# Performance work log

Hardware: AMD Instinct MI355X
Metric: run time of the kernel (lower is better)

The kernel has to match this reference:

```python
import jax, jax.numpy as jnp
import numpy as np

DIM = 128
N_VAR = 100000
N_CON = 100000
N_NODES = 200000
N_EDGES = 640000


def setup_inputs() -> dict:
    key = jax.random.key(0)
    ks = jax.random.split(key, 25)
    d = DIM
    u = lambda k, s: jax.random.uniform(k, s, jnp.float32, -0.1, 0.1)
    inp = {
        "var_node_features": jax.random.normal(ks[0], (N_VAR, 2), jnp.float32),
        "con_node_features": jax.random.normal(ks[1], (N_CON, 2), jnp.float32),
        "node_types": jax.random.randint(ks[2], (N_NODES,), 0, 2),
        "assoc_var": jnp.arange(N_VAR),
        "assoc_con": N_VAR + jnp.arange(N_CON),
        "edge_index": jax.random.randint(ks[3], (2, N_EDGES), 0, N_NODES),
        "edge_types": jax.random.randint(ks[4], (N_EDGES,), 0, 2),
        "edge_features": jax.random.normal(ks[5], (N_EDGES, 1), jnp.float32),
        "var_w1": u(ks[6], (2, d)), "var_b1": u(ks[7], (d,)),
        "var_w2": u(ks[8], (d, d)), "var_b2": u(ks[9], (d,)),
        "con_w1": u(ks[10], (2, d)), "con_b1": u(ks[11], (d,)),
        "con_w2": u(ks[12], (d, d)), "con_b2": u(ks[13], (d,)),
    }
    for i, k0 in zip((1, 2, 3), (14, 17, 20)):
        inp[f"basis{i}"] = u(ks[k0], (1, d, d))      # num_bases=1
        inp[f"att{i}"] = u(ks[k0 + 1], (2, 1))       # num_relations=2
        inp[f"root{i}"] = u(ks[k0 + 2], (d, d))
        inp[f"bias{i}"] = jnp.zeros((d,), jnp.float32)
    inp["fc1_w"] = u(ks[23], (4 * d, d))
    inp["fc1_b"] = jnp.zeros((d,), jnp.float32)
    inp["fc4_w"] = u(ks[24], (d, 1))
    inp["fc4_b"] = jnp.zeros((1,), jnp.float32)
    return inp


def rgcn(x, src, dst, etype, basis, att, root, bias):
    # basis: [1, d, d], att: [2, 1] -> per-relation weights [2, d, d]
    d = x.shape[-1]
    w = (att @ basis.reshape(basis.shape[0], -1)).reshape(2, d, d)
    xj = x[src]  # [E, d] gather
    # only 2 relations: two GEMMs + select (avoids [E,d,d] materialization)
    msg = jnp.where((etype == 0)[:, None], xj @ w[0], xj @ w[1])
    s = jax.ops.segment_sum(msg, dst, num_segments=N_NODES)
    cnt = jax.ops.segment_sum(jnp.ones((dst.shape[0],), x.dtype), dst, num_segments=N_NODES)
    agg = s / jnp.maximum(cnt, 1.0)[:, None]  # mean aggregation
    return agg + x @ root + bias


def reference(var_node_features, con_node_features, node_types, assoc_var, assoc_con,
              edge_index, edge_types, edge_features,
              var_w1, var_b1, var_w2, var_b2,
              con_w1, con_b1, con_w2, con_b2,
              basis1, att1, root1, bias1,
              basis2, att2, root2, bias2,
              basis3, att3, root3, bias3,
              fc1_w, fc1_b, fc4_w, fc4_b):
    n = jnp.maximum(var_node_features @ var_w1 + var_b1, 0.0) @ var_w2 + var_b2
    e = jnp.maximum(con_node_features @ con_w1 + con_b1, 0.0) @ con_w2 + con_b2
    x = jnp.zeros((node_types.shape[0], n.shape[-1]), n.dtype)
    x = x.at[assoc_var].set(n).at[assoc_con].set(e)
    src, dst = edge_index[0], edge_index[1]
    x1 = jax.nn.relu(rgcn(x, src, dst, edge_types, basis1, att1, root1, bias1))
    x2 = jax.nn.relu(rgcn(x1, src, dst, edge_types, basis2, att2, root2, bias2))
    x3 = jax.nn.relu(rgcn(x2, src, dst, edge_types, basis3, att3, root3, bias3))
    h = jnp.concatenate([x, x1, x2, x3], axis=-1)[assoc_var]  # [n_var, 4d]
    h = jax.nn.relu(h @ fc1_w + fc1_b)
    # dropout p=0.5 is identity in eval mode
    return (h @ fc4_w + fc4_b)[:, 0]
```

## Files before the change

kernel.cpp:

```cpp
#include <hip/hip_runtime.h>
#include <hip/hip_bf16.h>

#define D 128
#define NV 100000
#define NC 100000
#define NN 200000
#define NE 640000

typedef __attribute__((ext_vector_type(4))) float f32x4;
typedef __attribute__((ext_vector_type(8))) short bf16x8;

static __device__ __forceinline__ unsigned short f2b(float f) {
    __hip_bfloat16 h = __float2bfloat16(f);
    union { __hip_bfloat16 h; unsigned short u; } c; c.h = h; return c.u;
}
static __device__ __forceinline__ float b2f(unsigned short b) {
    union { unsigned int u; float f; } c; c.u = ((unsigned int)b) << 16; return c.f;
}

template<bool RELU>
static __device__ __forceinline__ void split8v(const float f[8], bf16x8& ah, bf16x8& al)
{
    union { unsigned short s[8]; bf16x8 v; } ph, pl;
    #pragma unroll
    for (int j = 0; j < 8; ++j) {
        float x = RELU ? fmaxf(f[j], 0.f) : f[j];
        ph.s[j] = f2b(x);
        pl.s[j] = f2b(x - b2f(ph.s[j]));
    }
    ah = ph.v; al = pl.v;
}

union H8 { _Float16 h[8]; uint4 u; };
union H4 { _Float16 h[4]; uint2 u; };

struct PrepArgs { const float* src[12]; };

__global__ __launch_bounds__(256, 1) void prep_kernel(PrepArgs a, unsigned short* wt)
{
    const float* W = a.src[blockIdx.y];
    unsigned short* hi = wt + (size_t)blockIdx.y * 32768;
    unsigned short* lo = hi + 16384;
    const int o = blockIdx.x * 1024 + threadIdx.x * 4;
    const int slice = o >> 10;
    const int n     = (o >> 3) & 127;
    const int j0    = o & 7;
    union { unsigned short s[4]; unsigned long long u; } ph, pl;
    #pragma unroll
    for (int i = 0; i < 4; ++i) {
        const int k = slice * 8 + j0 + i;
        const float w = W[k * 128 + n];
        ph.s[i] = f2b(w);
        pl.s[i] = f2b(w - b2f(ph.s[i]));
    }
    *(unsigned long long*)&hi[o] = ph.u;
    *(unsigned long long*)&lo[o] = pl.u;
}

static __device__ __forceinline__ const bf16x8* wfrag(const unsigned short* wt,
                                                      int ks, int lg, int n)
{
    return (const bf16x8*)(wt + (((ks * 4 + lg) * 128) + n) * 8);
}

static __device__ __forceinline__ char* haddr(char* base, int row, int byteoff)
{
    return base + row * 256 + (byteoff ^ ((row & 7) << 4));
}

template<bool RELU, bool HASAGG>
static __device__ __forceinline__ void wsplit8(uint4 xv, uint4 gv,
                                               char* hb, char* lb, int srow, int ob0)
{
    H8 a0; a0.u = xv;
    float f[8];
    #pragma unroll
    for (int j = 0; j < 8; ++j) f[j] = (float)a0.h[j];
    if (HASAGG) {
        H8 g0; g0.u = gv;
        #pragma unroll
        for (int j = 0; j < 8; ++j) f[j] += (float)g0.h[j];
    }
    bf16x8 h0, l0;
    split8v<RELU>(f, h0, l0);
    *(bf16x8*)(hb + srow * 256 + ob0) = h0;
    *(bf16x8*)(lb + srow * 256 + ob0) = l0;
}

template<int AMODE, bool RELU_A, bool ADD_C>
__global__ __launch_bounds__(256, 4) void gemm6(
    const void* A, const _Float16* __restrict__ agg,
    const float* __restrict__ w1, const float* __restrict__ b1, int M,
    const unsigned short* __restrict__ wt, const float* __restrict__ bias,
    _Float16* Cout)
{
    __shared__ unsigned short Hs[2][2][32 * 128];
    const int tid  = threadIdx.x;
    const int lane = tid & 63, wv = tid >> 6;
    const int li   = lane & 15, lg = lane >> 4;
    const int colbase = wv * 32;

    bf16x8 bh[4][2], bl[4][2];
    #pragma unroll
    for (int ks = 0; ks < 4; ++ks)
        #pragma unroll
        for (int nf = 0; nf < 2; ++nf) {
            const int n = colbase + nf * 16 + li;
            bh[ks][nf] = *wfrag(wt,         ks, lg, n);
            bl[ks][nf] = *wfrag(wt + 16384, ks, lg, n);
        }

    const int ntiles = (M + 31) / 32;
    const int G = gridDim.x;
    const int t0 = blockIdx.x;
    if (t0 >= ntiles) return;

    const int srow = tid >> 3;
    const int skf  = (tid & 7) * 16;
    const int sw   = (srow & 7) << 4;
    const int ob0  = (skf * 2) ^ sw;
    const int ob1  = (skf * 2 + 16) ^ sw;

    #define LOADT(TT, XV0, XV1, GV0, GV1, FV)                                    \
    {                                                                            \
        int grow = (TT) * 32 + srow; if (grow >= M) grow = M - 1;                \
        if (AMODE == 2) {                                                        \
            FV = *(const float2*)((const float*)A + (size_t)grow * 2);           \
        } else {                                                                 \
            const uint4* ap = (const uint4*)((const _Float16*)A + (size_t)grow * D + skf); \
            XV0 = ap[0]; XV1 = ap[1];                                            \
            if (AMODE == 1) {                                                    \
                const uint4* gp = (const uint4*)(agg + (size_t)grow * D + skf);  \
                GV0 = gp[0]; GV1 = gp[1];                                        \
            }                                                                    \
        }                                                                        \
    }
    #define WRITET(BUF, XV0, XV1, GV0, GV1, FV)                                  \
    {                                                                            \
        char* hb_ = (char*)&Hs[BUF][0][0];                                       \
        char* lb_ = (char*)&Hs[BUF][1][0];                                       \
        if (AMODE == 2) {                                                        \
            float f[16];                                                         \
            const float f0 = FV.x, f1 = FV.y;                                    \
            _Pragma("unroll")                                                    \
            for (int q = 0; q < 4; ++q) {                                        \
                const float4 wa = *(const float4*)(w1 + skf + q * 4);            \
                const float4 wb = *(const float4*)(w1 + 128 + skf + q * 4);      \
                const float4 bb = *(const float4*)(b1 + skf + q * 4);            \
                f[q*4+0] = fmaxf(fmaf(f0, wa.x, fmaf(f1, wb.x, bb.x)), 0.f);     \
                f[q*4+1] = fmaxf(fmaf(f0, wa.y, fmaf(f1, wb.y, bb.y)), 0.f);     \
                f[q*4+2] = fmaxf(fmaf(f0, wa.z, fmaf(f1, wb.z, bb.z)), 0.f);     \
                f[q*4+3] = fmaxf(fmaf(f0, wa.w, fmaf(f1, wb.w, bb.w)), 0.f);     \
            }                                                                    \
            bf16x8 h0, l0, h1, l1;                                               \
            split8v<RELU_A>(&f[0], h0, l0);                                     \
            split8v<RELU_A>(&f[8], h1, l1);                                     \
            char* hbr = hb_ + srow * 256; char* lbr = lb_ + srow * 256;          \
            *(bf16x8*)(hbr + ob0) = h0; *(bf16x8*)(hbr + ob1) = h1;              \
            *(bf16x8*)(lbr + ob0) = l0; *(bf16x8*)(lbr + ob1) = l1;              \
        } else {                                                                 \
            wsplit8<RELU_A, AMODE == 1>(XV0, GV0, hb_, lb_, srow, ob0);          \
            wsplit8<RELU_A, AMODE == 1>(XV1, GV1, hb_, lb_, srow, ob1);          \
        }                                                                        \
    }

    {
        uint4 xv0 = {0,0,0,0}, xv1 = {0,0,0,0}, gv0 = {0,0,0,0}, gv1 = {0,0,0,0};
        float2 fv = {0, 0};
        LOADT(t0, xv0, xv1, gv0, gv1, fv);
        WRITET(0, xv0, xv1, gv0, gv1, fv);
    }
    __syncthreads();

    int cur = 0;
    for (int t = t0; t < ntiles; t += G) {
        const int tn = t + G;
        const bool pf = tn < ntiles;
        uint4 xv0 = {0,0,0,0}, xv1 = {0,0,0,0}, gv0 = {0,0,0,0}, gv1 = {0,0,0,0};
        float2 fv = {0, 0};
        if (pf) LOADT(tn, xv0, xv1, gv0, gv1, fv);

        char* hb = (char*)&Hs[cur][0][0];
        char* lb = (char*)&Hs[cur][1][0];
        f32x4 acc[2][2];
        #pragma unroll
        for (int ms = 0; ms < 2; ++ms)
            #pragma unroll
            for (int nf = 0; nf < 2; ++nf) acc[ms][nf] = (f32x4){0.f, 0.f, 0.f, 0.f};
        #pragma unroll
        for (int ks = 0; ks < 4; ++ks) {
            const int kb = ks * 64 + lg * 16;
            bf16x8 ah[2], al[2];
            #pragma unroll
            for (int ms = 0; ms < 2; ++ms) {
                const int row = ms * 16 + li;
                ah[ms] = *(const bf16x8*)haddr(hb, row, kb);
                al[ms] = *(const bf16x8*)haddr(lb, row, kb);
            }
            #pragma unroll
            for (int nf = 0; nf < 2; ++nf)
                #pragma unroll
                for (int ms = 0; ms < 2; ++ms) {
                    acc[ms][nf] = __builtin_amdgcn_mfma_f32_16x16x32_bf16(bh[ks][nf], ah[ms], acc[ms][nf], 0, 0, 0);
                    acc[ms][nf] = __builtin_amdgcn_mfma_f32_16x16x32_bf16(bh[ks][nf], al[ms], acc[ms][nf], 0, 0, 0);
                    acc[ms][nf] = __builtin_amdgcn_mfma_f32_16x16x32_bf16(bl[ks][nf], ah[ms], acc[ms][nf], 0, 0, 0);
                }
        }

        #pragma unroll
        for (int ms = 0; ms < 2; ++ms) {
            const int grow = t * 32 + ms * 16 + li;
            if (grow < M) {
                _Float16* crow = Cout + (size_t)grow * D;
                #pragma unroll
                for (int nf = 0; nf < 2; ++nf) {
                    const int c0 = colbase + nf * 16 + lg * 4;
                    float v[4];
                    #pragma unroll
                    for (int r = 0; r < 4; ++r) v[r] = acc[ms][nf][r];
                    if (bias) {
                        const float4 b = *(const float4*)(bias + c0);
                        v[0] += b.x; v[1] += b.y; v[2] += b.z; v[3] += b.w;
                    }
                    if (ADD_C) {
                        H4 rd; rd.u = *(const uint2*)(crow + c0);
                        #pragma unroll
                        for (int r = 0; r < 4; ++r) v[r] += (float)rd.h[r];
                    }
                    H4 pk;
                    #pragma unroll
                    for (int r = 0; r < 4; ++r) pk.h[r] = (_Float16)v[r];
                    *(uint2*)(crow + c0) = pk.u;
                }
            }
        }

        if (pf) WRITET(cur ^ 1, xv0, xv1, gv0, gv1, fv);
        __syncthreads();
        cur ^= 1;
    }
    #undef LOADT
    #undef WRITET
}

__global__ __launch_bounds__(256, 4) void ugemmf(
    const _Float16* __restrict__ x, const _Float16* __restrict__ agg,
    const _Float16* __restrict__ u, int M,
    const unsigned short* __restrict__ wt,
    const float* __restrict__ fc1_b, const float* __restrict__ fc4_w,
    const float* __restrict__ fc4_b, float* __restrict__ out)
{
    __shared__ unsigned short Hs[2][2][32 * 128];
    const int tid  = threadIdx.x;
    const int lane = tid & 63, wv = tid >> 6;
    const int li   = lane & 15, lg = lane >> 4;
    const int colbase = wv * 32;
    const float fb40 = fc4_b[0];

    bf16x8 bh[4][2], bl[4][2];
    #pragma unroll
    for (int ks = 0; ks < 4; ++ks)
        #pragma unroll
        for (int nf = 0; nf < 2; ++nf) {
            const int n = colbase + nf * 16 + li;
            bh[ks][nf] = *wfrag(wt,         ks, lg, n);
            bl[ks][nf] = *wfrag(wt + 16384, ks, lg, n);
        }

    const int ntiles = (M + 31) / 32;
    const int G = gridDim.x;
    const int t0 = blockIdx.x;
    if (t0 >= ntiles) return;

    const int srow = tid >> 3;
    const int skf  = (tid & 7) * 16;
    const int sw   = (srow & 7) << 4;
    const int ob0  = (skf * 2) ^ sw;
    const int ob1  = (skf * 2 + 16) ^ sw;

    #define LOADU(TT, XV0, XV1, GV0, GV1)                                        \
    {                                                                            \
        int grow = (TT) * 32 + srow; if (grow >= M) grow = M - 1;                \
        const uint4* ap = (const uint4*)(x + (size_t)grow * D + skf);            \
        XV0 = ap[0]; XV1 = ap[1];                                                \
        const uint4* gp = (const uint4*)(agg + (size_t)grow * D + skf);          \
        GV0 = gp[0]; GV1 = gp[1];                                                \
    }

    {
        uint4 xv0, xv1, gv0, gv1;
        LOADU(t0, xv0, xv1, gv0, gv1);
        wsplit8<true, true>(xv0, gv0, (char*)&Hs[0][0][0], (char*)&Hs[0][1][0], srow, ob0);
        wsplit8<true, true>(xv1, gv1, (char*)&Hs[0][0][0], (char*)&Hs[0][1][0], srow, ob1);
    }
    __syncthreads();

    int cur = 0;
    for (int t = t0; t < ntiles; t += G) {
        const int tn = t + G;
        const bool pf = tn < ntiles;
        uint4 xv0 = {0,0,0,0}, xv1 = {0,0,0,0}, gv0 = {0,0,0,0}, gv1 = {0,0,0,0};
        if (pf) LOADU(tn, xv0, xv1, gv0, gv1);

        char* hb = (char*)&Hs[cur][0][0];
        char* lb = (char*)&Hs[cur][1][0];
        f32x4 acc[2][2];
        #pragma unroll
        for (int ms = 0; ms < 2; ++ms)
            #pragma unroll
            for (int nf = 0; nf < 2; ++nf) acc[ms][nf] = (f32x4){0.f, 0.f, 0.f, 0.f};
        #pragma unroll
        for (int ks = 0; ks < 4; ++ks) {
            const int kb = ks * 64 + lg * 16;
            bf16x8 ah[2], al[2];
            #pragma unroll
            for (int ms = 0; ms < 2; ++ms) {
                const int row = ms * 16 + li;
                ah[ms] = *(const bf16x8*)haddr(hb, row, kb);
                al[ms] = *(const bf16x8*)haddr(lb, row, kb);
            }
            #pragma unroll
            for (int nf = 0; nf < 2; ++nf)
                #pragma unroll
                for (int ms = 0; ms < 2; ++ms) {
                    acc[ms][nf] = __builtin_amdgcn_mfma_f32_16x16x32_bf16(bh[ks][nf], ah[ms], acc[ms][nf], 0, 0, 0);
                    acc[ms][nf] = __builtin_amdgcn_mfma_f32_16x16x32_bf16(bh[ks][nf], al[ms], acc[ms][nf], 0, 0, 0);
                    acc[ms][nf] = __builtin_amdgcn_mfma_f32_16x16x32_bf16(bl[ks][nf], ah[ms], acc[ms][nf], 0, 0, 0);
                }
        }

        #pragma unroll
        for (int ms = 0; ms < 2; ++ms) {
            const int grow = t * 32 + ms * 16 + li;
            float s = 0.f;
            if (grow < M) {
                const _Float16* urow = u + (size_t)grow * D;
                #pragma unroll
                for (int nf = 0; nf < 2; ++nf) {
                    const int c0 = colbase + nf * 16 + lg * 4;
                    const float4 fb = *(const float4*)(fc1_b + c0);
                    const float4 fw = *(const float4*)(fc4_w + c0);
                    H4 rd; rd.u = *(const uint2*)(urow + c0);
                    const float fbv[4] = {fb.x, fb.y, fb.z, fb.w};
                    const float fwv[4] = {fw.x, fw.y, fw.z, fw.w};
                    #pragma unroll
                    for (int r = 0; r < 4; ++r) {
                        const float v = acc[ms][nf][r] + (float)rd.h[r] + fbv[r];
                        s += fmaxf(v, 0.f) * fwv[r];
                    }
                }
            }
            s += __shfl_xor(s, 16);
            s += __shfl_xor(s, 32);
            if (lg == 0 && grow < M) {
                const float add = s + ((wv == 0) ? fb40 : 0.f);
                atomicAdd(out + grow, add);
            }
        }

        if (pf) {
            wsplit8<true, true>(xv0, gv0, (char*)&Hs[cur ^ 1][0][0],
                                (char*)&Hs[cur ^ 1][1][0], srow, ob0);
            wsplit8<true, true>(xv1, gv1, (char*)&Hs[cur ^ 1][0][0],
                                (char*)&Hs[cur ^ 1][1][0], srow, ob1);
        }
        __syncthreads();
        cur ^= 1;
    }
    #undef LOADU
}

template<bool RELU_A, bool HASAGG, bool UADD>
__global__ __launch_bounds__(768, 3) void layer6(
    _Float16* x, const _Float16* __restrict__ agg, int M, int Mroot,
    const unsigned short* __restrict__ wtb, const unsigned short* __restrict__ wtr,
    const unsigned short* __restrict__ wtu, const float* __restrict__ bias,
    unsigned short* __restrict__ y, _Float16* __restrict__ u, int Mu)
{
    __shared__ unsigned short Hs[2][2][32 * 128];
    const int tid  = threadIdx.x;
    const int lane = tid & 63, wv = tid >> 6;
    const int li   = lane & 15, lg = lane >> 4;
    const int wgrp = wv >> 2;
    const int colbase = (wv & 3) * 32;
    const unsigned short* wsel = (wgrp == 0) ? wtb : (wgrp == 1) ? wtr : wtu;

    bf16x8 bh[4][2], bl[4][2];
    #pragma unroll
    for (int ks = 0; ks < 4; ++ks)
        #pragma unroll
        for (int nf = 0; nf < 2; ++nf) {
            const int n = colbase + nf * 16 + li;
            bh[ks][nf] = *wfrag(wsel,         ks, lg, n);
            bl[ks][nf] = *wfrag(wsel + 16384, ks, lg, n);
        }
    float4 bv[2] = {{0,0,0,0},{0,0,0,0}};
    if (wgrp == 1) {
        bv[0] = *(const float4*)(bias + colbase + 0  + lg * 4);
        bv[1] = *(const float4*)(bias + colbase + 16 + lg * 4);
    }

    const int ntiles = (M + 31) / 32;
    const int G = gridDim.x;
    const int t0 = blockIdx.x;
    if (t0 >= ntiles) return;

    const bool stager = tid < 512;
    const int srow = (tid & 511) >> 4;
    const int skf  = (tid & 15) * 8;
    const int sw   = (srow & 7) << 4;
    const int ob0  = (skf * 2) ^ sw;

    if (stager) {
        int grow = t0 * 32 + srow; if (grow >= M) grow = M - 1;
        uint4 xv = *(const uint4*)(x + (size_t)grow * D + skf);
        uint4 gv = {0,0,0,0};
        if (HASAGG) gv = *(const uint4*)(agg + (size_t)grow * D + skf);
        wsplit8<RELU_A, HASAGG>(xv, gv, (char*)&Hs[0][0][0], (char*)&Hs[0][1][0], srow, ob0);
    }
    __syncthreads();

    int cur = 0;
    for (int t = t0; t < ntiles; t += G) {
        const int tn = t + G;
        const bool pf = stager && (tn < ntiles);
        uint4 xv = {0,0,0,0}, gv = {0,0,0,0};
        if (pf) {
            int grow = tn * 32 + srow; if (grow >= M) grow = M - 1;
            xv = *(const uint4*)(x + (size_t)grow * D + skf);
            if (HASAGG) gv = *(const uint4*)(agg + (size_t)grow * D + skf);
        }

        char* hb = (char*)&Hs[cur][0][0];
        char* lb = (char*)&Hs[cur][1][0];
        f32x4 acc[2][2];
        #pragma unroll
        for (int ms = 0; ms < 2; ++ms)
            #pragma unroll
            for (int nf = 0; nf < 2; ++nf) acc[ms][nf] = (f32x4){0.f, 0.f, 0.f, 0.f};
        #pragma unroll
        for (int ks = 0; ks < 4; ++ks) {
            const int kb = ks * 64 + lg * 16;
            bf16x8 ah[2], al[2];
            #pragma unroll
            for (int ms = 0; ms < 2; ++ms) {
                const int row = ms * 16 + li;
                ah[ms] = *(const bf16x8*)haddr(hb, row, kb);
                al[ms] = *(const bf16x8*)haddr(lb, row, kb);
            }
            #pragma unroll
            for (int nf = 0; nf < 2; ++nf)
                #pragma unroll
                for (int ms = 0; ms < 2; ++ms) {
                    acc[ms][nf] = __builtin_amdgcn_mfma_f32_16x16x32_bf16(bh[ks][nf], ah[ms], acc[ms][nf], 0, 0, 0);
                    acc[ms][nf] = __builtin_amdgcn_mfma_f32_16x16x32_bf16(bh[ks][nf], al[ms], acc[ms][nf], 0, 0, 0);
                    acc[ms][nf] = __builtin_amdgcn_mfma_f32_16x16x32_bf16(bl[ks][nf], ah[ms], acc[ms][nf], 0, 0, 0);
                }
        }

        #pragma unroll
        for (int ms = 0; ms < 2; ++ms) {
            const int grow = t * 32 + ms * 16 + li;
            if (wgrp == 0) {
                if (grow < M) {
                    unsigned short* yrow = y + (size_t)grow * D;
                    #pragma unroll
                    for (int nf = 0; nf < 2; ++nf) {
                        const int c0 = colbase + nf * 16 + lg * 4;
                        union { unsigned short s[4]; uint2 v; } pk;
                        #pragma unroll
                        for (int r = 0; r < 4; ++r) pk.s[r] = f2b(acc[ms][nf][r]);
                        *(uint2*)(yrow + c0) = pk.v;
                    }
                }
            } else if (wgrp == 1) {
                if (grow < Mroot) {
                    _Float16* xrow = x + (size_t)grow * D;
                    #pragma unroll
                    for (int nf = 0; nf < 2; ++nf) {
                        const int c0 = colbase + nf * 16 + lg * 4;
                        const float bb[4] = {bv[nf].x, bv[nf].y, bv[nf].z, bv[nf].w};
                        H4 pk;
                        #pragma unroll
                        for (int r = 0; r < 4; ++r) pk.h[r] = (_Float16)(acc[ms][nf][r] + bb[r]);
                        *(uint2*)(xrow + c0) = pk.u;
                    }
                }
            } else {
                if (grow < Mu) {
                    _Float16* urow = u + (size_t)grow * D;
                    #pragma unroll
                    for (int nf = 0; nf < 2; ++nf) {
                        const int c0 = colbase + nf * 16 + lg * 4;
                        float v[4];
                        #pragma unroll
                        for (int r = 0; r < 4; ++r) v[r] = acc[ms][nf][r];
                        if (UADD) {
                            H4 rd; rd.u = *(const uint2*)(urow + c0);
                            #pragma unroll
                            for (int r = 0; r < 4; ++r) v[r] += (float)rd.h[r];
                        }
                        H4 pk;
                        #pragma unroll
                        for (int r = 0; r < 4; ++r) pk.h[r] = (_Float16)v[r];
                        *(uint2*)(urow + c0) = pk.u;
                    }
                }
            }
        }

        if (pf)
            wsplit8<RELU_A, HASAGG>(xv, gv, (char*)&Hs[cur ^ 1][0][0],
                                    (char*)&Hs[cur ^ 1][1][0], srow, ob0);
        __syncthreads();
        cur ^= 1;
    }
}

__global__ void hist_kernel(const int* __restrict__ dst, int* __restrict__ deg, int ne)
{
    int g = blockIdx.x * blockDim.x + threadIdx.x;
    if (g < ne) atomicAdd(&deg[dst[g]], 1);
}

__global__ __launch_bounds__(256, 1) void scan_blk(int* __restrict__ buf,
                                                   int* __restrict__ sums, int n)
{
    __shared__ int part[256];
    const int tid  = threadIdx.x;
    const int base = blockIdx.x * 1024 + tid * 4;
    int v0 = (base + 0 < n) ? buf[base + 0] : 0;
    int v1 = (base + 1 < n) ? buf[base + 1] : 0;
    int v2 = (base + 2 < n) ? buf[base + 2] : 0;
    int v3 = (base + 3 < n) ? buf[base + 3] : 0;
    const int t0 = v0, t1 = t0 + v1, t2 = t1 + v2, t3 = t2 + v3;
    part[tid] = t3;
    __syncthreads();
    #pragma unroll
    for (int off = 1; off < 256; off <<= 1) {
        int x = part[tid];
        if (tid >= off) x += part[tid - off];
        __syncthreads();
        part[tid] = x;
        __syncthreads();
    }
    if (tid == 255) sums[blockIdx.x] = part[255];
    const int excl = tid ? part[tid - 1] : 0;
    if (base + 0 < n) buf[base + 0] = excl;
    if (base + 1 < n) buf[base + 1] = excl + t0;
    if (base + 2 < n) buf[base + 2] = excl + t1;
    if (base + 3 < n) buf[base + 3] = excl + t2;
}

__global__ __launch_bounds__(256, 1) void scan_top(int* __restrict__ sums, int nb)
{
    __shared__ int part[256];
    const int tid = threadIdx.x;
    part[tid] = (tid < nb) ? sums[tid] : 0;
    __syncthreads();
    #pragma unroll
    for (int off = 1; off < 256; off <<= 1) {
        int x = part[tid];
        if (tid >= off) x += part[tid - off];
        __syncthreads();
        part[tid] = x;
        __syncthreads();
    }
    if (tid < nb) sums[tid] = tid ? part[tid - 1] : 0;
}

__global__ void scan_add(int* __restrict__ buf, const int* __restrict__ sums, int n)
{
    int i = blockIdx.x * blockDim.x + threadIdx.x;
    if (i < n) buf[i] += sums[i >> 10];
}

__global__ void fill_kernel(const int* __restrict__ src, const int* __restrict__ dst,
                            const int* __restrict__ etype,
                            int* __restrict__ cursor, int* __restrict__ edges, int ne)
{
    int e = blockIdx.x * blockDim.x + threadIdx.x;
    if (e < ne) {
        const int pos = atomicAdd(&cursor[dst[e]], 1);
        edges[pos] = (src[e] << 1) | (etype[e] & 1);
    }
}

__global__ __launch_bounds__(256, 2) void gather_agg(
    const int* __restrict__ cursor, const int* __restrict__ edges,
    const float* __restrict__ att, const unsigned short* __restrict__ y,
    _Float16* __restrict__ agg, int nn)
{
    const int gid  = blockIdx.x * 256 + threadIdx.x;
    const int node = gid >> 4;
    const int l    = gid & 15;
    if (node >= nn) return;
    const int end   = cursor[node];
    const int start = node ? cursor[node - 1] : 0;
    const float a0 = att[0], a1 = att[1];
    float s0[8] = {0,0,0,0,0,0,0,0}, s1[8] = {0,0,0,0,0,0,0,0};
    int j = start;
    for (; j + 2 <= end; j += 2) {
        const int p0 = edges[j], p1 = edges[j + 1];
        const float w0 = (p0 & 1) ? a1 : a0;
        const float w1 = (p1 & 1) ? a1 : a0;
        const uint4 va = ((const uint4*)(y + ((size_t)(p0 >> 1)) * D))[l];
        const uint4 vb = ((const uint4*)(y + ((size_t)(p1 >> 1)) * D))[l];
        const unsigned int wa[4] = {va.x, va.y, va.z, va.w};
        const unsigned int wb[4] = {vb.x, vb.y, vb.z, vb.w};
        #pragma unroll
        for (int q = 0; q < 4; ++q) {
            s0[q * 2 + 0] = fmaf(w0, b2f((unsigned short)(wa[q] & 0xFFFF)), s0[q * 2 + 0]);
            s0[q * 2 + 1] = fmaf(w0, b2f((unsigned short)(wa[q] >> 16)),    s0[q * 2 + 1]);
            s1[q * 2 + 0] = fmaf(w1, b2f((unsigned short)(wb[q] & 0xFFFF)), s1[q * 2 + 0]);
            s1[q * 2 + 1] = fmaf(w1, b2f((unsigned short)(wb[q] >> 16)),    s1[q * 2 + 1]);
        }
    }
    if (j < end) {
        const int p0 = edges[j];
        const float w0 = (p0 & 1) ? a1 : a0;
        const uint4 va = ((const uint4*)(y + ((size_t)(p0 >> 1)) * D))[l];
        const unsigned int wa[4] = {va.x, va.y, va.z, va.w};
        #pragma unroll
        for (int q = 0; q < 4; ++q) {
            s0[q * 2 + 0] = fmaf(w0, b2f((unsigned short)(wa[q] & 0xFFFF)), s0[q * 2 + 0]);
            s0[q * 2 + 1] = fmaf(w0, b2f((unsigned short)(wa[q] >> 16)),    s0[q * 2 + 1]);
        }
    }
    const float inv = 1.0f / fmaxf((float)(end - start), 1.0f);
    H8 o;
    #pragma unroll
    for (int q = 0; q < 8; ++q) o.h[q] = (_Float16)((s0[q] + s1[q]) * inv);
    *(uint4*)(agg + (size_t)node * D + l * 8) = o.u;
}

extern "C" void kernel_launch(void* const* d_in, const int* in_sizes, int n_in,
                              void* d_out, int out_size, void* d_ws, size_t ws_size,
                              hipStream_t stream)
{
    const float* varf      = (const float*)d_in[0];
    const float* conf      = (const float*)d_in[1];
    const int*   edge_src  = (const int*)d_in[5];
    const int*   edge_dst  = edge_src + NE;
    const int*   etype     = (const int*)d_in[6];
    const float* var_w1 = (const float*)d_in[8];
    const float* var_b1 = (const float*)d_in[9];
    const float* var_w2 = (const float*)d_in[10];
    const float* var_b2 = (const float*)d_in[11];
    const float* con_w1 = (const float*)d_in[12];
    const float* con_b1 = (const float*)d_in[13];
    const float* con_w2 = (const float*)d_in[14];
    const float* con_b2 = (const float*)d_in[15];
    const float* basisL[3] = {(const float*)d_in[16], (const float*)d_in[20], (const float*)d_in[24]};
    const float* attL[3]   = {(const float*)d_in[17], (const float*)d_in[21], (const float*)d_in[25]};
    const float* rootL[3]  = {(const float*)d_in[18], (const float*)d_in[22], (const float*)d_in[26]};
    const float* biasL[3]  = {(const float*)d_in[19], (const float*)d_in[23], (const float*)d_in[27]};
    const float* fc1_w = (const float*)d_in[28];
    const float* fc1_b = (const float*)d_in[29];
    const float* fc4_w = (const float*)d_in[30];
    const float* fc4_b = (const float*)d_in[31];

    const size_t XB  = (size_t)NN * D * 2;
    const size_t YB  = (size_t)NN * D * 2;
    const size_t AB  = (size_t)NN * D * 2;
    const size_t UB  = (size_t)NV * D * 2;
    const size_t CUR = (size_t)NN * 4;
    const size_t EDG = (size_t)NE * 4;
    const size_t SUM = 4096;
    const size_t WT  = (size_t)12 * 32768 * 2;
    const size_t need = XB + YB + AB + UB + CUR + EDG + SUM + WT;
    if (ws_size < need) {
        hipMemsetAsync(d_out, 0, (size_t)out_size * sizeof(float), stream);
        return;
    }
    char* p = (char*)d_ws;
    _Float16*       x      = (_Float16*)p;       p += XB;
    unsigned short* y      = (unsigned short*)p; p += YB;
    _Float16*       agg    = (_Float16*)p;       p += AB;
    _Float16*       u      = (_Float16*)p;       p += UB;
    int*            cursor = (int*)p;            p += CUR;
    int*            edges  = (int*)p;            p += EDG;
    int*            sums   = (int*)p;            p += SUM;
    unsigned short* wt     = (unsigned short*)p;

    hipMemsetAsync(d_out, 0, (size_t)out_size * sizeof(float), stream);

    PrepArgs pa;
    pa.src[0] = basisL[0]; pa.src[1] = basisL[1]; pa.src[2] = basisL[2];
    pa.src[3] = rootL[0];  pa.src[4] = rootL[1];  pa.src[5] = rootL[2];
    pa.src[6] = fc1_w;                 pa.src[7] = fc1_w + 128 * 128;
    pa.src[8] = fc1_w + 2 * 128 * 128; pa.src[9] = fc1_w + 3 * 128 * 128;
    pa.src[10] = var_w2;               pa.src[11] = con_w2;
    prep_kernel<<<dim3(16, 12), 256, 0, stream>>>(pa, wt);

    hipMemsetAsync(cursor, 0, CUR, stream);
    hist_kernel<<<(NE + 255) / 256, 256, 0, stream>>>(edge_dst, cursor, NE);
    const int nblk = (NN + 1023) / 1024;
    scan_blk<<<nblk, 256, 0, stream>>>(cursor, sums, NN);
    scan_top<<<1, 256, 0, stream>>>(sums, nblk);
    scan_add<<<(NN + 255) / 256, 256, 0, stream>>>(cursor, sums, NN);
    fill_kernel<<<(NE + 255) / 256, 256, 0, stream>>>(edge_src, edge_dst, etype,
                                                      cursor, edges, NE);

    const int GM = 1024;
    const int GL = 256;

    gemm6<2, false, false><<<GM, 256, 0, stream>>>(
        varf, nullptr, var_w1, var_b1, NV, wt + (size_t)10 * 32768, var_b2, x);
    gemm6<2, false, false><<<GM, 256, 0, stream>>>(
        conf, nullptr, con_w1, con_b1, NC, wt + (size_t)11 * 32768, con_b2,
        x + (size_t)NV * D);

    for (int l = 0; l < 3; ++l) {
        const unsigned short* wb_ = wt + (size_t)l * 32768;
        const unsigned short* wr_ = wt + (size_t)(3 + l) * 32768;
        const unsigned short* wu_ = wt + (size_t)(6 + l) * 32768;
        const int mroot = (l == 2) ? NV : NN;
        const int gn    = (l == 2) ? NV : NN;
        if (l == 0)
            layer6<false, false, false><<<GL, 768, 0, stream>>>(
                x, nullptr, NN, mroot, wb_, wr_, wu_, biasL[0], y, u, NV);
        else
            layer6<true, true, true><<<GL, 768, 0, stream>>>(
                x, agg, NN, mroot, wb_, wr_, wu_, biasL[l], y, u, NV);
        gather_agg<<<(gn * 16 + 255) / 256, 256, 0, stream>>>(
            cursor, edges, attL[l], y, agg, gn);
    }

    ugemmf<<<GM, 256, 0, stream>>>(x, agg, u, NV, wt + (size_t)9 * 32768,
                                   fc1_b, fc4_w, fc4_b, (float*)d_out);
}
```

Before: 415.7 us.

## Widen per-wave column tiles in layer kernel, shrink block, skip idle waves

The per-layer GEMM kernel now runs 384 threads (6 waves) per block instead of 768. Each wave covers 64 output columns with twice the resident weight fragments, and each staging thread loads two 16-byte chunks. Waves whose root or u output lies past Mroot/Mu now skip the MFMA work, which matters in layer 3 and for the u group. The grid grows from 256 to 1024 blocks. The aim is better A-tile reuse per LDS read and less wasted compute, at the cost of more registers per wave and possible occupancy loss.

```diff
diff --git a/kernel.cpp b/kernel.cpp
--- a/kernel.cpp
+++ b/kernel.cpp
@@ -371,7 +371,7 @@
 }
 
 template<bool RELU_A, bool HASAGG, bool UADD>
-__global__ __launch_bounds__(768, 3) void layer6(
+__global__ __launch_bounds__(384, 6) void layer10(
     _Float16* x, const _Float16* __restrict__ agg, int M, int Mroot,
     const unsigned short* __restrict__ wtb, const unsigned short* __restrict__ wtr,
     const unsigned short* __restrict__ wtu, const float* __restrict__ bias,
@@ -381,23 +381,24 @@
     const int tid  = threadIdx.x;
     const int lane = tid & 63, wv = tid >> 6;
     const int li   = lane & 15, lg = lane >> 4;
-    const int wgrp = wv >> 2;
-    const int colbase = (wv & 3) * 32;
+    const int wgrp = wv >> 1;
+    const int colbase = (wv & 1) * 64;
     const unsigned short* wsel = (wgrp == 0) ? wtb : (wgrp == 1) ? wtr : wtu;
 
-    bf16x8 bh[4][2], bl[4][2];
+    bf16x8 bh[4][4], bl[4][4];
     #pragma unroll
     for (int ks = 0; ks < 4; ++ks)
         #pragma unroll
-        for (int nf = 0; nf < 2; ++nf) {
+        for (int nf = 0; nf < 4; ++nf) {
             const int n = colbase + nf * 16 + li;
             bh[ks][nf] = *wfrag(wsel,         ks, lg, n);
             bl[ks][nf] = *wfrag(wsel + 16384, ks, lg, n);
         }
-    float4 bv[2] = {{0,0,0,0},{0,0,0,0}};
+    float4 bv[4] = {{0,0,0,0},{0,0,0,0},{0,0,0,0},{0,0,0,0}};
     if (wgrp == 1) {
-        bv[0] = *(const float4*)(bias + colbase + 0  + lg * 4);
-        bv[1] = *(const float4*)(bias + colbase + 16 + lg * 4);
+        #pragma unroll
+        for (int nf = 0; nf < 4; ++nf)
+            bv[nf] = *(const float4*)(bias + colbase + nf * 16 + lg * 4);
     }
 
     const int ntiles = (M + 31) / 32;
@@ -405,18 +406,24 @@
     const int t0 = blockIdx.x;
     if (t0 >= ntiles) return;
 
-    const bool stager = tid < 512;
-    const int srow = (tid & 511) >> 4;
-    const int skf  = (tid & 15) * 8;
+    const bool stager = tid < 256;
+    const int srow = (tid & 255) >> 3;
+    const int skf  = (tid & 7) * 16;
     const int sw   = (srow & 7) << 4;
     const int ob0  = (skf * 2) ^ sw;
+    const int ob1  = (skf * 2 + 16) ^ sw;
 
     if (stager) {
         int grow = t0 * 32 + srow; if (grow >= M) grow = M - 1;
-        uint4 xv = *(const uint4*)(x + (size_t)grow * D + skf);
-        uint4 gv = {0,0,0,0};
-        if (HASAGG) gv = *(const uint4*)(agg + (size_t)grow * D + skf);
-        wsplit8<RELU_A, HASAGG>(xv, gv, (char*)&Hs[0][0][0], (char*)&Hs[0][1][0], srow, ob0);
+        const uint4* ap = (const uint4*)(x + (size_t)grow * D + skf);
+        uint4 xv0 = ap[0], xv1 = ap[1];
+        uint4 gv0 = {0,0,0,0}, gv1 = {0,0,0,0};
+        if (HASAGG) {
+            const uint4* gp = (const uint4*)(agg + (size_t)grow * D + skf);
+            gv0 = gp[0]; gv1 = gp[1];
+        }
+        wsplit8<RELU_A, HASAGG>(xv0, gv0, (char*)&Hs[0][0][0], (char*)&Hs[0][1][0], srow, ob0);
+        wsplit8<RELU_A, HASAGG>(xv1, gv1, (char*)&Hs[0][0][0], (char*)&Hs[0][1][0], srow, ob1);
     }
     __syncthreads();
 
@@ -424,94 +431,105 @@
     for (int t = t0; t < ntiles; t += G) {
         const int tn = t + G;
         const bool pf = stager && (tn < ntiles);
-        uint4 xv = {0,0,0,0}, gv = {0,0,0,0};
+        uint4 xv0 = {0,0,0,0}, xv1 = {0,0,0,0}, gv0 = {0,0,0,0}, gv1 = {0,0,0,0};
         if (pf) {
             int grow = tn * 32 + srow; if (grow >= M) grow = M - 1;
-            xv = *(const uint4*)(x + (size_t)grow * D + skf);
-            if (HASAGG) gv = *(const uint4*)(agg + (size_t)grow * D + skf);
-        }
-
-        char* hb = (char*)&Hs[cur][0][0];
-        char* lb = (char*)&Hs[cur][1][0];
-        f32x4 acc[2][2];
-        #pragma unroll
-        for (int ms = 0; ms < 2; ++ms)
-            #pragma unroll
-            for (int nf = 0; nf < 2; ++nf) acc[ms][nf] = (f32x4){0.f, 0.f, 0.f, 0.f};
-        #pragma unroll
-        for (int ks = 0; ks < 4; ++ks) {
-            const int kb = ks * 64 + lg * 16;
-            bf16x8 ah[2], al[2];
-            #pragma unroll
-            for (int ms = 0; ms < 2; ++ms) {
-                const int row = ms * 16 + li;
-                ah[ms] = *(const bf16x8*)haddr(hb, row, kb);
-                al[ms] = *(const bf16x8*)haddr(lb, row, kb);
+            const uint4* ap = (const uint4*)(x + (size_t)grow * D + skf);
+            xv0 = ap[0]; xv1 = ap[1];
+            if (HASAGG) {
+                const uint4* gp = (const uint4*)(agg + (size_t)grow * D + skf);
+                gv0 = gp[0]; gv1 = gp[1];
             }
-            #pragma unroll
-            for (int nf = 0; nf < 2; ++nf)
+        }
+
+        const bool dowork = (wgrp == 0) ||
+                            (wgrp == 1 ? (t * 32 < Mroot) : (t * 32 < Mu));
+        if (dowork) {
+            char* hb = (char*)&Hs[cur][0][0];
+            char* lb = (char*)&Hs[cur][1][0];
+            f32x4 acc[2][4];
+            #pragma unroll
+            for (int ms = 0; ms < 2; ++ms)
+                #pragma unroll
+                for (int nf = 0; nf < 4; ++nf) acc[ms][nf] = (f32x4){0.f, 0.f, 0.f, 0.f};
+            #pragma unroll
+            for (int ks = 0; ks < 4; ++ks) {
+                const int kb = ks * 64 + lg * 16;
+                bf16x8 ah[2], al[2];
                 #pragma unroll
                 for (int ms = 0; ms < 2; ++ms) {
-                    acc[ms][nf] = __builtin_amdgcn_mfma_f32_16x16x32_bf16(bh[ks][nf], ah[ms], acc[ms][nf], 0, 0, 0);
-                    acc[ms][nf] = __builtin_amdgcn_mfma_f32_16x16x32_bf16(bh[ks][nf], al[ms], acc[ms][nf], 0, 0, 0);
-                    acc[ms][nf] = __builtin_amdgcn_mfma_f32_16x16x32_bf16(bl[ks][nf], ah[ms], acc[ms][nf], 0, 0, 0);
+                    const int row = ms * 16 + li;
+                    ah[ms] = *(const bf16x8*)haddr(hb, row, kb);
+                    al[ms] = *(const bf16x8*)haddr(lb, row, kb);
                 }
-        }
-
-        #pragma unroll
-        for (int ms = 0; ms < 2; ++ms) {
-            const int grow = t * 32 + ms * 16 + li;
-            if (wgrp == 0) {
-                if (grow < M) {
-                    unsigned short* yrow = y + (size_t)grow * D;
+                #pragma unroll
+                for (int nf = 0; nf < 4; ++nf)
                     #pragma unroll
-                    for (int nf = 0; nf < 2; ++nf) {
-                        const int c0 = colbase + nf * 16 + lg * 4;
-                        union { unsigned short s[4]; uint2 v; } pk;
+                    for (int ms = 0; ms < 2; ++ms) {
+                        acc[ms][nf] = __builtin_amdgcn_mfma_f32_16x16x32_bf16(bh[ks][nf], ah[ms], acc[ms][nf], 0, 0, 0);
+                        acc[ms][nf] = __builtin_amdgcn_mfma_f32_16x16x32_bf16(bh[ks][nf], al[ms], acc[ms][nf], 0, 0, 0);
+                        acc[ms][nf] = __builtin_amdgcn_mfma_f32_16x16x32_bf16(bl[ks][nf], ah[ms], acc[ms][nf], 0, 0, 0);
+                    }
+            }
+
+            #pragma unroll
+            for (int ms = 0; ms < 2; ++ms) {
+                const int gr = t * 32 + ms * 16 + li;
+                if (wgrp == 0) {
+                    if (gr < M) {
+                        unsigned short* yrow = y + (size_t)gr * D;
                         #pragma unroll
-                        for (int r = 0; r < 4; ++r) pk.s[r] = f2b(acc[ms][nf][r]);
-                        *(uint2*)(yrow + c0) = pk.v;
+                        for (int nf = 0; nf < 4; ++nf) {
+                            const int c0 = colbase + nf * 16 + lg * 4;
+                            union { unsigned short s[4]; uint2 v; } pk;
+                            #pragma unroll
+                            for (int r = 0; r < 4; ++r) pk.s[r] = f2b(acc[ms][nf][r]);
+                            *(uint2*)(yrow + c0) = pk.v;
+                        }
                     }
-                }
-            } else if (wgrp == 1) {
-                if (grow < Mroot) {
-                    _Float16* xrow = x + (size_t)grow * D;
-                    #pragma unroll
-                    for (int nf = 0; nf < 2; ++nf) {
-                        const int c0 = colbase + nf * 16 + lg * 4;
-                        const float bb[4] = {bv[nf].x, bv[nf].y, bv[nf].z, bv[nf].w};
-                        H4 pk;
+                } else if (wgrp == 1) {
+                    if (gr < Mroot) {
+                        _Float16* xrow = x + (size_t)gr * D;
                         #pragma unroll
-                        for (int r = 0; r < 4; ++r) pk.h[r] = (_Float16)(acc[ms][nf][r] + bb[r]);
-                        *(uint2*)(xrow + c0) = pk.u;
+                        for (int nf = 0; nf < 4; ++nf) {
+                            const int c0 = colbase + nf * 16 + lg * 4;
+                            const float bb[4] = {bv[nf].x, bv[nf].y, bv[nf].z, bv[nf].w};
+                            H4 pk;
+                            #pragma unroll
+                            for (int r = 0; r < 4; ++r) pk.h[r] = (_Float16)(acc[ms][nf][r] + bb[r]);
+                            *(uint2*)(xrow + c0) = pk.u;
+                        }
                     }
-                }
-            } else {
-                if (grow < Mu) {
-                    _Float16* urow = u + (size_t)grow * D;
-                    #pragma unroll
-                    for (int nf = 0; nf < 2; ++nf) {
-                        const int c0 = colbase + nf * 16 + lg * 4;
-                        float v[4];
+                } else {
+                    if (gr < Mu) {
+                        _Float16* urow = u + (size_t)gr * D;
                         #pragma unroll
-                        for (int r = 0; r < 4; ++r) v[r] = acc[ms][nf][r];
-                        if (UADD) {
-                            H4 rd; rd.u = *(const uint2*)(urow + c0);
+                        for (int nf = 0; nf < 4; ++nf) {
+                            const int c0 = colbase + nf * 16 + lg * 4;
+                            float v[4];
                             #pragma unroll
-                            for (int r = 0; r < 4; ++r) v[r] += (float)rd.h[r];
+                            for (int r = 0; r < 4; ++r) v[r] = acc[ms][nf][r];
+                            if (UADD) {
+                                H4 rd; rd.u = *(const uint2*)(urow + c0);
+                                #pragma unroll
+                                for (int r = 0; r < 4; ++r) v[r] += (float)rd.h[r];
+                            }
+                            H4 pk;
+                            #pragma unroll
+                            for (int r = 0; r < 4; ++r) pk.h[r] = (_Float16)v[r];
+                            *(uint2*)(urow + c0) = pk.u;
                         }
-                        H4 pk;
-                        #pragma unroll
-                        for (int r = 0; r < 4; ++r) pk.h[r] = (_Float16)v[r];
-                        *(uint2*)(urow + c0) = pk.u;
                     }
                 }
             }
         }
 
-        if (pf)
-            wsplit8<RELU_A, HASAGG>(xv, gv, (char*)&Hs[cur ^ 1][0][0],
+        if (pf) {
+            wsplit8<RELU_A, HASAGG>(xv0, gv0, (char*)&Hs[cur ^ 1][0][0],
                                     (char*)&Hs[cur ^ 1][1][0], srow, ob0);
+            wsplit8<RELU_A, HASAGG>(xv1, gv1, (char*)&Hs[cur ^ 1][0][0],
+                                    (char*)&Hs[cur ^ 1][1][0], srow, ob1);
+        }
         __syncthreads();
         cur ^= 1;
     }
@@ -703,7 +721,7 @@
                                                       cursor, edges, NE);
 
     const int GM = 1024;
-    const int GL = 256;
+    const int GL = 1024;
 
     gemm6<2, false, false><<<GM, 256, 0, stream>>>(
         varf, nullptr, var_w1, var_b1, NV, wt + (size_t)10 * 32768, var_b2, x);
@@ -718,10 +736,10 @@
         const int mroot = (l == 2) ? NV : NN;
         const int gn    = (l == 2) ? NV : NN;
         if (l == 0)
-            layer6<false, false, false><<<GL, 768, 0, stream>>>(
+            layer10<false, false, false><<<GL, 384, 0, stream>>>(
                 x, nullptr, NN, mroot, wb_, wr_, wu_, biasL[0], y, u, NV);
         else
-            layer6<true, true, true><<<GL, 768, 0, stream>>>(
+            layer10<true, true, true><<<GL, 384, 0, stream>>>(
                 x, agg, NN, mroot, wb_, wr_, wu_, biasL[l], y, u, NV);
         gather_agg<<<(gn * 16 + 255) / 256, 256, 0, stream>>>(
             cursor, edges, attL[l], y, agg, gn);
```

After: 1.366 ms. 3.29x slower.
